# Performance work log

Hardware: AMD Instinct MI355X
Metric: run time of the kernel (lower is better)

## Reference

```python
import jax, jax.numpy as jnp
import numpy as np

IMG_H, IMG_W = 832.0, 1472.0
PATCH = 32
NUM_CLASSES = 4
LAMBDA_BOX = 5.0
LAMBDA_CLS = 1.0
B, N, T = 512, 1176, 64


def setup_inputs() -> dict:
    key = jax.random.key(0)
    k1, k2, k3, k4, k5, k6 = jax.random.split(key, 6)
    predictions = jax.random.normal(k1, (B, N, 5 + NUM_CLASSES), dtype=jnp.float32)
    # build valid absolute-pixel target boxes (x1 < x2, y1 < y2)
    x1 = jax.random.uniform(k2, (B, T), dtype=jnp.float32) * (IMG_W - 260.0)
    y1 = jax.random.uniform(k3, (B, T), dtype=jnp.float32) * (IMG_H - 260.0)
    w = 16.0 + jax.random.uniform(k4, (B, T), dtype=jnp.float32) * 240.0
    h = 16.0 + jax.random.uniform(k5, (B, T), dtype=jnp.float32) * 240.0
    target_boxes = jnp.stack([x1, y1, x1 + w, y1 + h], axis=-1)  # (B,T,4)
    target_classes = jax.random.randint(k6, (B, T), 0, NUM_CLASSES, dtype=jnp.int32)
    return {"predictions": predictions, "target_boxes": target_boxes,
            "target_classes": target_classes}


def _decode_boxes(pred):
    # pred: (B,N,9) -> absolute corner boxes (B,N,4)
    cx = (pred[..., 0] * 2.0 - 1.0) * (IMG_W / 2.0)
    cy = (pred[..., 1] * 2.0 - 1.0) * (IMG_H / 2.0)
    w = jnp.exp(pred[..., 2]) * (IMG_W / (IMG_W // PATCH))  # stride 32
    h = jnp.exp(pred[..., 3]) * (IMG_H / (IMG_H // PATCH))
    return jnp.stack([cx - w / 2, cy - h / 2, cx + w / 2, cy + h / 2], axis=-1)


def _pairwise_iou(boxes, tgt):
    # boxes: (B,N,4), tgt: (B,T,4) -> (B,N,T)
    b = boxes[:, :, None, :]
    t = tgt[:, None, :, :]
    ix1 = jnp.maximum(b[..., 0], t[..., 0])
    iy1 = jnp.maximum(b[..., 1], t[..., 1])
    ix2 = jnp.minimum(b[..., 2], t[..., 2])
    iy2 = jnp.minimum(b[..., 3], t[..., 3])
    inter = jnp.maximum(ix2 - ix1, 0.0) * jnp.maximum(iy2 - iy1, 0.0)
    a1 = (b[..., 2] - b[..., 0]) * (b[..., 3] - b[..., 1])
    a2 = (t[..., 2] - t[..., 0]) * (t[..., 3] - t[..., 1])
    union = a1 + a2 - inter
    return jnp.where(union > 0, inter / jnp.where(union > 0, union, 1.0), 0.0)


def _smooth_l1_sum(a, b):
    d = jnp.abs(a - b)
    return jnp.sum(jnp.where(d < 1.0, 0.5 * d * d, d - 0.5))


def _bce_logits_sum(logits, targets):
    # sum of max(x,0) - x*t + log(1+exp(-|x|)) == logaddexp(0,x) - x*t
    return jnp.sum(jnp.logaddexp(0.0, logits) - logits * targets)


def reference(predictions, target_boxes, target_classes):
    batch = predictions.shape[0]
    boxes = _decode_boxes(predictions)                      # (B,N,4)
    ious = _pairwise_iou(jax.lax.stop_gradient(boxes), target_boxes)  # (B,N,T)
    matched = jnp.argmax(ious, axis=1)                      # (B,T) indices into N

    # positive mask via scatter (mirrors positive_mask[matched_preds] = True)
    batch_idx = jnp.arange(batch)[:, None]
    pos = jnp.zeros((batch, boxes.shape[1]), jnp.float32).at[batch_idx, matched].set(1.0)

    # box loss (SmoothL1, sum)
    pred_matched = jnp.take_along_axis(boxes, matched[..., None], axis=1)  # (B,T,4)
    box_loss = _smooth_l1_sum(pred_matched, target_boxes)

    # class loss (CrossEntropy, sum)
    cls_logits_all = predictions[..., 5:5 + NUM_CLASSES]    # (B,N,C)
    cls_logits = jnp.take_along_axis(
        cls_logits_all, matched[..., None], axis=1)          # (B,T,C)
    logp = jax.nn.log_softmax(cls_logits, axis=-1)
    cls_loss = -jnp.sum(jnp.take_along_axis(
        logp, target_classes[..., None].astype(jnp.int32), axis=-1))

    # confidence loss (BCEWithLogits, sum) over all predictions
    conf_loss = _bce_logits_sum(predictions[..., 4], pos)

    total = LAMBDA_BOX * box_loss + LAMBDA_CLS * cls_loss + conf_loss
    return total / batch
```

## Files before the change

kernel.cpp:

```cpp
#include <hip/hip_runtime.h>

#define BATCH   512
#define NPRED   1176
#define NTGT    64
#define PRED_C  9
#define THREADS 512
#define NWAVE   8
#define WCHUNK  147
#define SEGCAP  148
#define NMASKW  ((NPRED + 31) / 32)
#define INVALID 0xFFFF

__global__ __launch_bounds__(THREADS) void det_loss_main(
    const float* __restrict__ pred,
    const float* __restrict__ tbox,
    const int*   __restrict__ tcls,
    float* __restrict__ partial)
{
    __shared__ float4 cbox[NWAVE * SEGCAP];
    __shared__ float  carea[NWAVE * SEGCAP];
    __shared__ unsigned short cidx[NWAVE * SEGCAP];
    __shared__ float4 stgt[NTGT];
    __shared__ float  slogit[NPRED];
    __shared__ unsigned int smask[NMASKW];
    __shared__ float  sbint[THREADS];
    __shared__ float  sbuni[THREADS];
    __shared__ unsigned short sbslot[THREADS];
    __shared__ float  shull[4];
    __shared__ float  sred[NWAVE];

    const int b   = blockIdx.x;
    const int tid = threadIdx.x;
    const int wv  = tid >> 6, ln = tid & 63;
    const float* pb = pred + (size_t)b * NPRED * PRED_C;

    if (tid < NMASKW) smask[tid] = 0u;

    if (tid < NTGT) {
        float4 tb = *reinterpret_cast<const float4*>(
            tbox + ((size_t)b * NTGT + tid) * 4);
        stgt[tid] = tb;
        float x1 = tb.x, y1 = tb.y, x2 = tb.z, y2 = tb.w;
        for (int off = 32; off > 0; off >>= 1) {
            x1 = fminf(x1, __shfl_xor(x1, off));
            y1 = fminf(y1, __shfl_xor(y1, off));
            x2 = fmaxf(x2, __shfl_xor(x2, off));
            y2 = fmaxf(y2, __shfl_xor(y2, off));
        }
        if (tid == 0) {
            shull[0] = x1; shull[1] = y1; shull[2] = x2; shull[3] = y2;
        }
    }
    __syncthreads();

    const float hx1 = shull[0], hy1 = shull[1];
    const float hx2 = shull[2], hy2 = shull[3];

    float s_conf = 0.f;
    int wcount = 0;
    const int n0 = wv * WCHUNK;
    for (int i = 0; i < 3; ++i) {
        int r = i * 64 + ln;
        int n = n0 + r;
        bool keep = false;
        float4 bb; float area = 0.f;
        if (r < WCHUNK) {
            const float* p = pb + n * PRED_C;
            float p0 = p[0], p1 = p[1], p2 = p[2], p3 = p[3], p4 = p[4];
            float cx = (p0 * 2.f - 1.f) * 736.f;
            float cy = (p1 * 2.f - 1.f) * 416.f;
            float w  = expf(p2) * 32.f;
            float h  = expf(p3) * 32.f;
            bb = make_float4(cx - 0.5f * w, cy - 0.5f * h,
                             cx + 0.5f * w, cy + 0.5f * h);
            area = w * h;
            slogit[n] = p4;
            s_conf += fmaxf(p4, 0.f) + log1pf(expf(-fabsf(p4)));
            keep = (bb.x < hx2) & (bb.z > hx1) & (bb.y < hy2) & (bb.w > hy1);
        }
        unsigned long long m = __ballot(keep);
        if (keep) {
            int pos  = wcount + __popcll(m & ((1ull << ln) - 1ull));
            int slot = wv * SEGCAP + pos;
            cbox[slot]  = bb;
            carea[slot] = area;
            cidx[slot]  = (unsigned short)n;
        }
        wcount += __popcll(m);
    }
    __syncthreads();

    {
        float4 tb = stgt[ln];
        float a2 = (tb.z - tb.x) * (tb.w - tb.y);
        float binter = 0.f, buni = 1.f;
        int   bslot = INVALID;
        const int base = wv * SEGCAP;
        for (int j = 0; j < wcount; ++j) {
            float4 bb = cbox[base + j];
            float a1  = carea[base + j];
            float ix1 = fmaxf(bb.x, tb.x);
            float iy1 = fmaxf(bb.y, tb.y);
            float ix2 = fminf(bb.z, tb.z);
            float iy2 = fminf(bb.w, tb.w);
            float iw  = fmaxf(ix2 - ix1, 0.f);
            float ih  = fmaxf(iy2 - iy1, 0.f);
            float inter = iw * ih;
            float uni   = (a1 + a2) - inter;
            bool better = inter * buni > binter * uni;
            binter = better ? inter : binter;
            buni   = better ? uni   : buni;
            bslot  = better ? (base + j) : bslot;
        }
        sbint[tid] = binter; sbuni[tid] = buni;
        sbslot[tid] = (unsigned short)bslot;
    }
    __syncthreads();

    float s_box = 0.f, s_cls = 0.f;
    if (tid < NTGT) {
        float binter = sbint[tid], buni = sbuni[tid];
        int   bslot = sbslot[tid];
        for (int w = 1; w < NWAVE; ++w) {
            float ci = sbint[w * 64 + tid];
            float cu = sbuni[w * 64 + tid];
            bool better = ci * buni > binter * cu;
            binter = better ? ci : binter;
            buni   = better ? cu : buni;
            bslot  = better ? sbslot[w * 64 + tid] : bslot;
        }
        int m; float4 pbx;
        if (bslot == INVALID) {
            m = 0;
            float p0 = pb[0], p1 = pb[1], p2 = pb[2], p3 = pb[3];
            float cx = (p0 * 2.f - 1.f) * 736.f;
            float cy = (p1 * 2.f - 1.f) * 416.f;
            float w  = expf(p2) * 32.f;
            float h  = expf(p3) * 32.f;
            pbx = make_float4(cx - 0.5f * w, cy - 0.5f * h,
                              cx + 0.5f * w, cy + 0.5f * h);
        } else {
            m = cidx[bslot];
            pbx = cbox[bslot];
        }
        atomicOr(&smask[m >> 5], 1u << (m & 31));

        float4 tb = stgt[tid];
        float d;
        d = fabsf(pbx.x - tb.x); s_box += (d < 1.f) ? 0.5f * d * d : d - 0.5f;
        d = fabsf(pbx.y - tb.y); s_box += (d < 1.f) ? 0.5f * d * d : d - 0.5f;
        d = fabsf(pbx.z - tb.z); s_box += (d < 1.f) ? 0.5f * d * d : d - 0.5f;
        d = fabsf(pbx.w - tb.w); s_box += (d < 1.f) ? 0.5f * d * d : d - 0.5f;

        const float* pc = pb + m * PRED_C + 5;
        float x0 = pc[0], x1 = pc[1], x2 = pc[2], x3 = pc[3];
        float mx = fmaxf(fmaxf(x0, x1), fmaxf(x2, x3));
        float se = expf(x0 - mx) + expf(x1 - mx) + expf(x2 - mx) + expf(x3 - mx);
        float lse = mx + logf(se);
        int tc = tcls[(size_t)b * NTGT + tid];
        float xt = (tc == 0) ? x0 : (tc == 1) ? x1 : (tc == 2) ? x2 : x3;
        s_cls += lse - xt;
    }
    __syncthreads();

    float s_pos = 0.f;
    for (int n = tid; n < NPRED; n += THREADS)
        if (smask[n >> 5] & (1u << (n & 31))) s_pos += slogit[n];

    float v = s_conf - s_pos + 5.f * s_box + s_cls;
    for (int off = 32; off > 0; off >>= 1)
        v += __shfl_down(v, off);
    if (ln == 0) sred[wv] = v;
    __syncthreads();
    if (tid == 0) {
        float t = 0.f;
        for (int i = 0; i < NWAVE; ++i) t += sred[i];
        partial[b] = t;
    }
}

__global__ __launch_bounds__(BATCH) void det_loss_final(
    const float* __restrict__ partial, float* __restrict__ out)
{
    int tid = threadIdx.x;
    float v = partial[tid];
    for (int off = 32; off > 0; off >>= 1)
        v += __shfl_down(v, off);
    __shared__ float s[8];
    if ((tid & 63) == 0) s[tid >> 6] = v;
    __syncthreads();
    if (tid == 0) {
        float t = 0.f;
        for (int i = 0; i < 8; ++i) t += s[i];
        *out = t * (1.f / BATCH);
    }
}

extern "C" void kernel_launch(void* const* d_in, const int* in_sizes, int n_in,
                              void* d_out, int out_size, void* d_ws, size_t ws_size,
                              hipStream_t stream) {
    const float* pred = (const float*)d_in[0];
    const float* tbox = (const float*)d_in[1];
    const int*   tcls = (const int*)d_in[2];
    float* out     = (float*)d_out;
    float* partial = (float*)d_ws;

    det_loss_main<<<BATCH, THREADS, 0, stream>>>(pred, tbox, tcls, partial);
    det_loss_final<<<1, BATCH, 0, stream>>>(partial, out);
}
```

Baseline: 15.48 us.

## Stage predictions in LDS coalesced and fuse final reduction via fixed-point atomics

Result: slower. 29.04 us (+87.5%).

```diff
diff --git a/kernel.cpp b/kernel.cpp
--- a/kernel.cpp
+++ b/kernel.cpp
@@ -7,16 +7,22 @@
 #define THREADS 512
 #define NWAVE   8
 #define WCHUNK  147
+#define WFLOATS (WCHUNK * PRED_C)
+#define SRAWP   1328
 #define SEGCAP  148
 #define NMASKW  ((NPRED + 31) / 32)
 #define INVALID 0xFFFF
+#define FIXSCALE 1048576.0
 
 __global__ __launch_bounds__(THREADS) void det_loss_main(
     const float* __restrict__ pred,
     const float* __restrict__ tbox,
     const int*   __restrict__ tcls,
-    float* __restrict__ partial)
+    unsigned long long* __restrict__ ws_sum,
+    unsigned int* __restrict__ ws_cnt,
+    float* __restrict__ out)
 {
+    __shared__ float  sraw[NWAVE * SRAWP];
     __shared__ float4 cbox[NWAVE * SEGCAP];
     __shared__ float  carea[NWAVE * SEGCAP];
     __shared__ unsigned short cidx[NWAVE * SEGCAP];
@@ -36,6 +42,16 @@
 
     if (tid < NMASKW) smask[tid] = 0u;
 
+    {
+        const float* src = pb + wv * WFLOATS;
+        float* dst = sraw + wv * SRAWP;
+        #pragma unroll
+        for (int k = 0; k < 21; ++k) {
+            int idx = k * 64 + ln;
+            if (idx < WFLOATS) dst[idx] = src[idx];
+        }
+    }
+
     if (tid < NTGT) {
         float4 tb = *reinterpret_cast<const float4*>(
             tbox + ((size_t)b * NTGT + tid) * 4);
@@ -59,13 +75,14 @@
     float s_conf = 0.f;
     int wcount = 0;
     const int n0 = wv * WCHUNK;
+    const float* wraw = sraw + wv * SRAWP;
     for (int i = 0; i < 3; ++i) {
         int r = i * 64 + ln;
         int n = n0 + r;
         bool keep = false;
         float4 bb; float area = 0.f;
         if (r < WCHUNK) {
-            const float* p = pb + n * PRED_C;
+            const float* p = wraw + r * PRED_C;
             float p0 = p[0], p1 = p[1], p2 = p[2], p3 = p[3], p4 = p[4];
             float cx = (p0 * 2.f - 1.f) * 736.f;
             float cy = (p1 * 2.f - 1.f) * 416.f;
@@ -132,7 +149,7 @@
         int m; float4 pbx;
         if (bslot == INVALID) {
             m = 0;
-            float p0 = pb[0], p1 = pb[1], p2 = pb[2], p3 = pb[3];
+            float p0 = sraw[0], p1 = sraw[1], p2 = sraw[2], p3 = sraw[3];
             float cx = (p0 * 2.f - 1.f) * 736.f;
             float cy = (p1 * 2.f - 1.f) * 416.f;
             float w  = expf(p2) * 32.f;
@@ -152,7 +169,8 @@
         d = fabsf(pbx.z - tb.z); s_box += (d < 1.f) ? 0.5f * d * d : d - 0.5f;
         d = fabsf(pbx.w - tb.w); s_box += (d < 1.f) ? 0.5f * d * d : d - 0.5f;
 
-        const float* pc = pb + m * PRED_C + 5;
+        const int mwv = m / WCHUNK, mr = m - mwv * WCHUNK;
+        const float* pc = sraw + mwv * SRAWP + mr * PRED_C + 5;
         float x0 = pc[0], x1 = pc[1], x2 = pc[2], x3 = pc[3];
         float mx = fmaxf(fmaxf(x0, x1), fmaxf(x2, x3));
         float se = expf(x0 - mx) + expf(x1 - mx) + expf(x2 - mx) + expf(x3 - mx);
@@ -175,24 +193,14 @@
     if (tid == 0) {
         float t = 0.f;
         for (int i = 0; i < NWAVE; ++i) t += sred[i];
-        partial[b] = t;
-    }
-}
-
-__global__ __launch_bounds__(BATCH) void det_loss_final(
-    const float* __restrict__ partial, float* __restrict__ out)
-{
-    int tid = threadIdx.x;
-    float v = partial[tid];
-    for (int off = 32; off > 0; off >>= 1)
-        v += __shfl_down(v, off);
-    __shared__ float s[8];
-    if ((tid & 63) == 0) s[tid >> 6] = v;
-    __syncthreads();
-    if (tid == 0) {
-        float t = 0.f;
-        for (int i = 0; i < 8; ++i) t += s[i];
-        *out = t * (1.f / BATCH);
+        long long q = llrint((double)t * FIXSCALE);
+        atomicAdd(ws_sum, (unsigned long long)q);
+        __threadfence();
+        unsigned int old = atomicAdd(ws_cnt, 1u);
+        if (old == BATCH - 1) {
+            unsigned long long s = atomicAdd(ws_sum, 0ull);
+            *out = (float)((double)(long long)s * (1.0 / (FIXSCALE * BATCH)));
+        }
     }
 }
 
@@ -202,9 +210,11 @@
     const float* pred = (const float*)d_in[0];
     const float* tbox = (const float*)d_in[1];
     const int*   tcls = (const int*)d_in[2];
-    float* out     = (float*)d_out;
-    float* partial = (float*)d_ws;
-
-    det_loss_main<<<BATCH, THREADS, 0, stream>>>(pred, tbox, tcls, partial);
-    det_loss_final<<<1, BATCH, 0, stream>>>(partial, out);
+    float* out = (float*)d_out;
+    unsigned long long* ws_sum = (unsigned long long*)d_ws;
+    unsigned int*       ws_cnt = (unsigned int*)((char*)d_ws + 8);
+
+    hipMemsetAsync(d_ws, 0, 16, stream);
+    det_loss_main<<<BATCH, THREADS, 0, stream>>>(pred, tbox, tcls,
+                                                 ws_sum, ws_cnt, out);
 }
```
